# Optimization experiments

Hardware: AMD Instinct MI355X
Metric: run time of the kernel (lower is better)

## Reference

```python
import jax, jax.numpy as jnp
import numpy as np
import math

B, LL, LP = 16, 256, 1024
HID, H = 128, 8
SCALE = math.sqrt(HID)


def setup_inputs() -> dict:
    key = jax.random.key(0)
    ks = jax.random.split(key, 20)
    s = 0.02
    inp = {
        "ligand": jax.random.normal(ks[0], (B, LL, HID), jnp.float32),
        "prot": jax.random.normal(ks[1], (B, LP, HID), jnp.float32),
        "inter": jax.random.uniform(ks[2], (B, 1, LL, LP), jnp.float32),
        # projection weights stored as [in, out] (x @ W + b)
        "Wl1": jax.random.normal(ks[3], (HID, HID * H), jnp.float32) * s,
        "bl1": jnp.zeros((HID * H,), jnp.float32),
        "Wl2": jax.random.normal(ks[4], (HID, HID * H), jnp.float32) * s,
        "bl2": jnp.zeros((HID * H,), jnp.float32),
        "Wp1": jax.random.normal(ks[5], (HID, HID * H), jnp.float32) * s,
        "bp1": jnp.zeros((HID * H,), jnp.float32),
        "Wp2": jax.random.normal(ks[6], (HID, HID * H), jnp.float32) * s,
        "bp2": jnp.zeros((HID * H,), jnp.float32),
        "W11": jax.random.normal(ks[7], (HID * H, HID), jnp.float32) * s,
        "b11": jnp.zeros((HID,), jnp.float32),
        "W12": jax.random.normal(ks[8], (2 * HID, HID), jnp.float32) * s,
        "b12": jnp.zeros((HID,), jnp.float32),
        "W21": jax.random.normal(ks[9], (HID * H, HID), jnp.float32) * s,
        "b21": jnp.zeros((HID,), jnp.float32),
        "W22": jax.random.normal(ks[10], (2 * HID, HID), jnp.float32) * s,
        "b22": jnp.zeros((HID,), jnp.float32),
    }
    return inp


def _heads(x):
    # [B, L, H*D] -> [B, H, L, D]
    b, l, _ = x.shape
    return x.reshape(b, l, H, HID).transpose(0, 2, 1, 3)


def reference(ligand, prot, inter, Wl1, bl1, Wl2, bl2, Wp1, bp1, Wp2, bp2,
              W11, b11, W12, b12, W21, b21, W22, b22):
    relu = jax.nn.relu
    l1 = _heads(relu(ligand @ Wl1 + bl1))   # [B,H,LL,D]
    l2 = _heads(relu(ligand @ Wl2 + bl2))   # [B,H,LL,D]
    p1 = _heads(relu(prot @ Wp1 + bp1))     # [B,H,LP,D]
    p2 = _heads(relu(prot @ Wp2 + bp2))     # [B,H,LP,D]

    energy = jnp.einsum('bhld,bhpd->bhlp', l1, p1) / SCALE
    att = jax.nn.softmax(energy * inter, axis=-1)  # dropout is identity at eval

    # ligand branch: att @ prot2 -> [B,LL,H*D]
    lig3 = jnp.einsum('bhlp,bhpd->blhd', att, p2).reshape(B, LL, H * HID)
    lig3 = jnp.concatenate([lig3 @ W11 + b11, ligand], axis=2)
    lig3 = relu(lig3 @ W12 + b12)

    # protein branch: att^T @ ligand2 -> [B,LP,H*D]
    prot3 = jnp.einsum('bhlp,bhld->bphd', att, l2).reshape(B, LP, H * HID)
    prot3 = jnp.concatenate([prot3 @ W21 + b21, prot], axis=2)
    prot3 = relu(prot3 @ W22 + b22)
    return (lig3, prot3)
```

## Files before the change

### kernel.cpp

```cpp
#include <hip/hip_runtime.h>
#include <hip/hip_bf16.h>

typedef unsigned short u16;
typedef __attribute__((ext_vector_type(4))) float f32x4;
typedef __attribute__((ext_vector_type(4))) unsigned int u32x4;
typedef __attribute__((ext_vector_type(4))) unsigned short u16x4;
typedef __attribute__((ext_vector_type(8))) unsigned short u16x8;
typedef __attribute__((ext_vector_type(8))) __bf16 bf16x8;

__device__ inline float u2f(u16 u) {
    union { unsigned int i; float f; } x; x.i = ((unsigned int)u) << 16; return x.f;
}
__device__ inline u16 f2u(float f) {
    __hip_bfloat16 b = __float2bfloat16(f);
    return *reinterpret_cast<u16*>(&b);
}
__device__ inline f32x4 mfma16(bf16x8 a, bf16x8 b, f32x4 c) {
    return __builtin_amdgcn_mfma_f32_16x16x32_bf16(a, b, c, 0, 0, 0);
}
__device__ inline void gload_lds16(const u16* g, u16* l) {
    __builtin_amdgcn_global_load_lds(
        (const __attribute__((address_space(1))) unsigned int*)g,
        (__attribute__((address_space(3))) unsigned int*)l, 16, 0, 0);
}

__global__ __launch_bounds__(256)
void proj_kernel(const u16* __restrict__ ligb, const u16* __restrict__ protb,
                 const u16* __restrict__ Wl1t, const u16* __restrict__ Wl2t,
                 const u16* __restrict__ Wp1t, const u16* __restrict__ Wp2t,
                 const float* __restrict__ bl1, const float* __restrict__ bl2,
                 const float* __restrict__ bp1, const float* __restrict__ bp2,
                 u16* __restrict__ l1v, u16* __restrict__ l2tv,
                 u16* __restrict__ p1v, u16* __restrict__ p2tv)
{
    __shared__ __align__(16) u16 As[128 * 64];
    __shared__ __align__(16) u16 Bs[128 * 64];
    const int y = blockIdx.y;
    const u16* A; const u16* B; const float* bias; u16* Out;
    int mode, logL, my;
    if (y < 32)       { A = ligb;  B = Wl1t; bias = bl1; Out = l1v;  mode = 1; logL = 8;  my = y; }
    else if (y < 64)  { A = ligb;  B = Wl2t; bias = bl2; Out = l2tv; mode = 3; logL = 8;  my = y - 32; }
    else if (y < 192) { A = protb; B = Wp1t; bias = bp1; Out = p1v;  mode = 1; logL = 10; my = y - 64; }
    else              { A = protb; B = Wp2t; bias = bp2; Out = p2tv; mode = 3; logL = 10; my = y - 192; }
    const int n0 = blockIdx.x * 128, m0 = my * 128;
    const int tid = threadIdx.x;
    const int w = tid >> 6, lane = tid & 63, q = lane >> 4, li = lane & 15;
    const int wr = w >> 1, wc = w & 1;

    const int srow = tid >> 3;
    const int cg = (tid & 7) ^ (srow & 7);
    const int ldsbase = ((tid >> 6) * 8) * 64;

    f32x4 acc[4][4];
    #pragma unroll
    for (int i = 0; i < 4; i++)
        #pragma unroll
        for (int j = 0; j < 4; j++) acc[i][j] = (f32x4){0.f, 0.f, 0.f, 0.f};

    #pragma unroll
    for (int kt = 0; kt < 128; kt += 64) {
        const u16* Ab = A + (long)m0 * 128 + kt + cg * 8;
        const u16* Bb = B + (long)n0 * 128 + kt + cg * 8;
        #pragma unroll
        for (int c = 0; c < 4; c++) {
            gload_lds16(Ab + (long)(c * 32 + srow) * 128, &As[ldsbase + c * 32 * 64]);
            gload_lds16(Bb + (long)(c * 32 + srow) * 128, &Bs[ldsbase + c * 32 * 64]);
        }
        __syncthreads();
        #pragma unroll
        for (int s = 0; s < 2; s++) {
            const int cp = ((s * 4 + q) ^ (li & 7)) * 8;
            bf16x8 av[4], bv[4];
            #pragma unroll
            for (int i = 0; i < 4; i++)
                av[i] = *(bf16x8*)&As[(wr * 64 + i * 16 + li) * 64 + cp];
            #pragma unroll
            for (int j = 0; j < 4; j++)
                bv[j] = *(bf16x8*)&Bs[(wc * 64 + j * 16 + li) * 64 + cp];
            #pragma unroll
            for (int i = 0; i < 4; i++)
                #pragma unroll
                for (int j = 0; j < 4; j++)
                    acc[i][j] = mfma16(av[i], bv[j], acc[i][j]);
        }
        __syncthreads();
    }

    const int Lm = (1 << logL) - 1;
    #pragma unroll
    for (int i = 0; i < 4; i++) {
        #pragma unroll
        for (int j = 0; j < 4; j++) {
            const int col = n0 + wc * 64 + j * 16 + li;
            const float bvs = bias[col];
            if (mode == 3) {
                const int row0 = m0 + wr * 64 + i * 16 + q * 4;
                long base = ((long)(((row0 >> logL) * 8 + (col >> 7)) * 128
                            + (col & 127)) << logL) + (row0 & Lm);
                u16x4 o;
                #pragma unroll
                for (int r = 0; r < 4; r++)
                    o[r] = f2u(fmaxf(acc[i][j][r] + bvs, 0.f));
                *(u16x4*)(Out + base) = o;
            } else {
                #pragma unroll
                for (int r = 0; r < 4; r++) {
                    const int row = m0 + wr * 64 + i * 16 + q * 4 + r;
                    long addr = ((long)((row >> logL) * 8 + (col >> 7)) << (logL + 7))
                              + ((long)(row & Lm) << 7) + (col & 127);
                    Out[addr] = f2u(fmaxf(acc[i][j][r] + bvs, 0.f));
                }
            }
        }
    }
}

__global__ __launch_bounds__(512)
void av_kernel(const u16* __restrict__ att, const u16* __restrict__ p2t,
               const u16* __restrict__ l2t,
               u16* __restrict__ lig3, u16* __restrict__ prot3)
{
    __shared__ __align__(16) u16 As[256 * 64];
    __shared__ __align__(16) u16 Bs[128 * 64];
    __shared__ __align__(16) u16 T[64 * 256];
    const int bid = blockIdx.x;
    const int tid = threadIdx.x;
    const int w = tid >> 6, lane = tid & 63, q = lane >> 4, li = lane & 15;
    const int wr = w >> 1, wc = w & 1;

    f32x4 acc[4][4];
    #pragma unroll
    for (int i = 0; i < 4; i++)
        #pragma unroll
        for (int j = 0; j < 4; j++) acc[i][j] = (f32x4){0.f, 0.f, 0.f, 0.f};

    if (bid < 128) {
        const int bh = bid;
        const u16* A = att + (long)bh * 262144;
        const u16* B = p2t + (long)bh * 131072;
        const int srow = tid >> 3;
        const int cg = (tid & 7) ^ (srow & 7);
        const int ldsbase = ((tid >> 6) * 8) * 64;

        for (int kt = 0; kt < 1024; kt += 64) {
            const u16* Ab = A + kt + cg * 8;
            const u16* Bb = B + kt + cg * 8;
            #pragma unroll
            for (int c = 0; c < 4; c++)
                gload_lds16(Ab + (long)(c * 64 + srow) * 1024,
                            &As[ldsbase + c * 64 * 64]);
            #pragma unroll
            for (int c = 0; c < 2; c++)
                gload_lds16(Bb + (long)(c * 64 + srow) * 1024,
                            &Bs[ldsbase + c * 64 * 64]);
            __syncthreads();
            #pragma unroll
            for (int s = 0; s < 2; s++) {
                const int cp = ((s * 4 + q) ^ (li & 7)) * 8;
                bf16x8 av[4], bv[4];
                #pragma unroll
                for (int i = 0; i < 4; i++)
                    av[i] = *(bf16x8*)&As[(wr * 64 + i * 16 + li) * 64 + cp];
                #pragma unroll
                for (int j = 0; j < 4; j++)
                    bv[j] = *(bf16x8*)&Bs[(wc * 64 + j * 16 + li) * 64 + cp];
                #pragma unroll
                for (int i = 0; i < 4; i++)
                    #pragma unroll
                    for (int j = 0; j < 4; j++)
                        acc[i][j] = mfma16(av[i], bv[j], acc[i][j]);
            }
            __syncthreads();
        }

        const long obase = ((long)(bh >> 3) * 256) * 1024 + (long)(bh & 7) * 128;
        #pragma unroll
        for (int i = 0; i < 4; i++)
            #pragma unroll
            for (int j = 0; j < 4; j++) {
                const int col = wc * 64 + j * 16 + li;
                #pragma unroll
                for (int r = 0; r < 4; r++) {
                    const int row = wr * 64 + i * 16 + q * 4 + r;
                    lig3[obase + (long)row * 1024 + col] = f2u(acc[i][j][r]);
                }
            }
    } else {
        const int pb = bid - 128;
        const int bh = pb >> 2;
        const int m0 = (pb & 3) * 256;
        const u16* A = att + (long)bh * 262144;
        const u16* B = l2t + (long)bh * 32768;
        const int w6 = tid >> 6;
        const int i5 = (tid >> 5) & 1;
        const int srow = tid >> 3;
        const int cg = (tid & 7) ^ (srow & 7);
        const int bldsbase = w6 * 8 * 64;

        for (int kt = 0; kt < 256; kt += 64) {
            #pragma unroll
            for (int c = 0; c < 4; c++) {
                gload_lds16(A + (long)(kt + w6 * 8 + c * 2 + i5) * 1024
                              + m0 + (tid & 31) * 8,
                            &T[w6 * 2048 + c * 512]);
            }
            #pragma unroll
            for (int c = 0; c < 2; c++)
                gload_lds16(B + (long)(c * 64 + srow) * 256 + kt + cg * 8,
                            &Bs[bldsbase + c * 64 * 64]);
            __syncthreads();

            #pragma unroll
            for (int pass = 0; pass < 4; pass++) {
                const int p = pass * 64 + (tid & 63);
                union { u16 e[8]; u32x4 v; } tmp;
                #pragma unroll
                for (int e = 0; e < 8; e++)
                    tmp.e[e] = T[(w6 * 8 + e) * 256 + p];
                *(u32x4*)&As[p * 64 + ((w6 ^ (p & 7)) * 8)] = tmp.v;
            }
            __syncthreads();

            #pragma unroll
            for (int s = 0; s < 2; s++) {
                const int cp = ((s * 4 + q) ^ (li & 7)) * 8;
                bf16x8 av[4], bv[4];
                #pragma unroll
                for (int i = 0; i < 4; i++)
                    av[i] = *(bf16x8*)&As[(wr * 64 + i * 16 + li) * 64 + cp];
                #pragma unroll
                for (int j = 0; j < 4; j++)
                    bv[j] = *(bf16x8*)&Bs[(wc * 64 + j * 16 + li) * 64 + cp];
                #pragma unroll
                for (int i = 0; i < 4; i++)
                    #pragma unroll
                    for (int j = 0; j < 4; j++)
                        acc[i][j] = mfma16(av[i], bv[j], acc[i][j]);
            }
            __syncthreads();
        }

        const long obase = ((long)(bh >> 3) * 1024 + m0) * 1024 + (long)(bh & 7) * 128;
        #pragma unroll
        for (int i = 0; i < 4; i++)
            #pragma unroll
            for (int j = 0; j < 4; j++) {
                const int col = wc * 64 + j * 16 + li;
                #pragma unroll
                for (int r = 0; r < 4; r++) {
                    const int row = wr * 64 + i * 16 + q * 4 + r;
                    prot3[obase + (long)row * 1024 + col] = f2u(acc[i][j][r]);
                }
            }
    }
}

__global__ __launch_bounds__(256)
void finals_kernel(const u16* __restrict__ lig3, const u16* __restrict__ ligb,
                   const u16* __restrict__ WstL, const float* __restrict__ bcL,
                   float* __restrict__ out0,
                   const u16* __restrict__ prot3, const u16* __restrict__ protb,
                   const u16* __restrict__ WstP, const float* __restrict__ bcP,
                   float* __restrict__ out1)
{
    __shared__ __align__(16) u16 As[128 * 64];
    __shared__ __align__(16) u16 Bs[128 * 64];
    const int y = blockIdx.y;
    const u16 *A, *A2, *B; const float* bias; float* Out; int my;
    if (y < 32) { A = lig3;  A2 = ligb;  B = WstL; bias = bcL; Out = out0; my = y; }
    else        { A = prot3; A2 = protb; B = WstP; bias = bcP; Out = out1; my = y - 32; }
    const int m0 = my * 128;
    const int tid = threadIdx.x;
    const int w = tid >> 6, lane = tid & 63, q = lane >> 4, li = lane & 15;
    const int wr = w >> 1, wc = w & 1;

    const int srow = tid >> 3;
    const int cg = (tid & 7) ^ (srow & 7);
    const int ldsbase = ((tid >> 6) * 8) * 64;

    f32x4 acc[4][4];
    #pragma unroll
    for (int i = 0; i < 4; i++)
        #pragma unroll
        for (int j = 0; j < 4; j++) acc[i][j] = (f32x4){0.f, 0.f, 0.f, 0.f};

    for (int kt = 0; kt < 1152; kt += 64) {
        const u16* Abase; long lda; int ktA;
        if (kt >= 1024) { Abase = A2; lda = 128; ktA = kt - 1024; }
        else            { Abase = A;  lda = 1024; ktA = kt; }
        const u16* Ab = Abase + (long)m0 * lda + ktA + cg * 8;
        const u16* Bb = B + kt + cg * 8;
        #pragma unroll
        for (int c = 0; c < 4; c++) {
            gload_lds16(Ab + (long)(c * 32 + srow) * lda,  &As[ldsbase + c * 32 * 64]);
            gload_lds16(Bb + (long)(c * 32 + srow) * 1152, &Bs[ldsbase + c * 32 * 64]);
        }
        __syncthreads();
        #pragma unroll
        for (int s = 0; s < 2; s++) {
            const int cp = ((s * 4 + q) ^ (li & 7)) * 8;
            bf16x8 av[4], bv[4];
            #pragma unroll
            for (int i = 0; i < 4; i++)
                av[i] = *(bf16x8*)&As[(wr * 64 + i * 16 + li) * 64 + cp];
            #pragma unroll
            for (int j = 0; j < 4; j++)
                bv[j] = *(bf16x8*)&Bs[(wc * 64 + j * 16 + li) * 64 + cp];
            #pragma unroll
            for (int i = 0; i < 4; i++)
                #pragma unroll
                for (int j = 0; j < 4; j++)
                    acc[i][j] = mfma16(av[i], bv[j], acc[i][j]);
        }
        __syncthreads();
    }

    #pragma unroll
    for (int i = 0; i < 4; i++)
        #pragma unroll
        for (int j = 0; j < 4; j++) {
            const int col = wc * 64 + j * 16 + li;
            const float bvs = bias[col];
            #pragma unroll
            for (int r = 0; r < 4; r++) {
                const int row = m0 + wr * 64 + i * 16 + q * 4 + r;
                Out[(long)row * 128 + col] = fmaxf(acc[i][j][r] + bvs, 0.f);
            }
        }
}

__global__ __launch_bounds__(512, 4)
void attn_kernel(const u16* __restrict__ l1, const u16* __restrict__ p1,
                 const u16* __restrict__ interb, u16* __restrict__ att)
{
    __shared__ __align__(16) u16 S[32 * 1024];
    __shared__ __align__(16) u16 Bs[2][64 * 64];
    const int id = blockIdx.x;
    const int bh = (id & 7) * 16 + (id >> 6);
    const int mt = (id >> 3) & 7;
    const int b  = bh >> 3;
    const int m0 = mt * 32;
    const int tid = threadIdx.x;
    const float rscale = 0.08838834764831845f;

    {
        const int w = tid >> 6, lane = tid & 63, q = lane >> 4, li = lane & 15;
        const int rgrp = w >> 2, pc = w & 3;
        const int srow = tid >> 3;
        const int cg = (tid & 7) ^ (srow & 7);
        bf16x8 af[4];
        const u16* lp = l1 + ((long)bh * 256 + m0 + rgrp * 16 + li) * 128 + q * 8;
        #pragma unroll
        for (int s = 0; s < 4; s++) af[s] = *(const bf16x8*)(lp + s * 32);
        const int sw = (rgrp * 4 + q) << 4;
        const u16* pbase = p1 + ((long)bh * 1024 + srow) * 128 + cg * 8;
        u16* ldst = &Bs[0][(tid >> 6) * 8 * 64];

        for (int pt = 0; pt < 16; pt++) {
            gload_lds16(pbase + (long)pt * 8192,      ldst);
            gload_lds16(pbase + (long)pt * 8192 + 64, ldst + 64 * 64);
            __syncthreads();
            f32x4 acc = (f32x4){0.f, 0.f, 0.f, 0.f};
            #pragma unroll
            for (int ks = 0; ks < 4; ks++) {
                bf16x8 bv = *(bf16x8*)&Bs[ks >> 1][(pc * 16 + li) * 64
                              + ((((ks & 1) * 4 + q) ^ (li & 7)) * 8)];
                acc = mfma16(af[ks], bv, acc);
            }
            const int col = pt * 64 + pc * 16 + li;
            const int lr0 = rgrp * 16 + q * 4;
            #pragma unroll
            for (int r = 0; r < 4; r++)
                S[((lr0 + r) << 10) + (col ^ sw)] = f2u(acc[r] * rscale);
            __syncthreads();
        }
    }

    const int row = tid >> 4;
    const int lj  = tid & 15;
    const int l   = m0 + row;
    const int sw2 = (row >> 2) << 4;
    const u16* ib = interb + ((long)b * 256 + l) * 1024;

    float mx = -1e30f;
    #pragma unroll
    for (int blk = 0; blk < 8; blk++) {
        const int c = blk * 128 + lj * 8;
        u16* sp = &S[(row << 10) + (c ^ sw2)];
        u16x8 s8 = *(u16x8*)sp;
        u16x8 i8 = *(const u16x8*)(ib + c);
        u16x8 o8;
        #pragma unroll
        for (int e = 0; e < 8; e++) {
            float v = u2f(s8[e]) * u2f(i8[e]);
            mx = fmaxf(mx, v);
            o8[e] = f2u(v);
        }
        *(u16x8*)sp = o8;
    }
    #pragma unroll
    for (int d = 1; d < 16; d <<= 1) mx = fmaxf(mx, __shfl_xor(mx, d, 64));

    float z = 0.f;
    #pragma unroll
    for (int blk = 0; blk < 8; blk++) {
        const int c = blk * 128 + lj * 8;
        u16x8 p8 = *(u16x8*)&S[(row << 10) + (c ^ sw2)];
        #pragma unroll
        for (int e = 0; e < 8; e++) z += __expf(u2f(p8[e]) - mx);
    }
    #pragma unroll
    for (int d = 1; d < 16; d <<= 1) z += __shfl_xor(z, d, 64);
    const float inv = 1.f / z;

    u16* op = att + ((long)bh * 256 + l) * 1024;
    #pragma unroll
    for (int blk = 0; blk < 8; blk++) {
        const int c = blk * 128 + lj * 8;
        u16x8 p8 = *(u16x8*)&S[(row << 10) + (c ^ sw2)];
        u16x8 o8;
        #pragma unroll
        for (int e = 0; e < 8; e++)
            o8[e] = f2u(__expf(u2f(p8[e]) - mx) * inv);
        *(u16x8*)(op + c) = o8;
    }
}

struct TPF { const float* src; u16* dst; int R; int C; };
struct TPF8 { TPF t[8]; };

__global__ __launch_bounds__(256)
void cvtw_kernel(TPF8 args)
{
    TPF tp = args.t[blockIdx.z];
    const int c0 = blockIdx.x * 32, r0 = blockIdx.y * 32;
    if (c0 >= tp.C || r0 >= tp.R) return;
    __shared__ u16 tile[32][33];
    const int tx = threadIdx.x & 31, ty = threadIdx.x >> 5;
    #pragma unroll
    for (int i = 0; i < 4; i++)
        tile[ty + i * 8][tx] = f2u(tp.src[(long)(r0 + ty + i * 8) * tp.C + c0 + tx]);
    __syncthreads();
    #pragma unroll
    for (int i = 0; i < 4; i++)
        tp.dst[(long)(c0 + ty + i * 8) * tp.R + r0 + tx] = tile[tx][ty + i * 8];
}

__global__ __launch_bounds__(256)
void wcomb_kernel(const u16* __restrict__ Wm0, const u16* __restrict__ Wo0,
                  const float* __restrict__ bm0, const float* __restrict__ bo0,
                  u16* __restrict__ Wst0, float* __restrict__ bc0,
                  const u16* __restrict__ Wm1, const u16* __restrict__ Wo1,
                  const float* __restrict__ bm1, const float* __restrict__ bo1,
                  u16* __restrict__ Wst1, float* __restrict__ bc1)
{
    const int zz = blockIdx.y;
    const u16* Wm = zz ? Wm1 : Wm0;
    const u16* Wo = zz ? Wo1 : Wo0;
    const float* bmid = zz ? bm1 : bm0;
    const float* bout = zz ? bo1 : bo0;
    u16* Wst = zz ? Wst1 : Wst0;
    float* bc = zz ? bc1 : bc0;
    const int n = blockIdx.x;
    const int tid = threadIdx.x;
    __shared__ float wrow[128];
    if (tid < 128) wrow[tid] = u2f(Wo[n * 256 + tid]);
    __syncthreads();
    for (int k = tid; k < 1024; k += 256) {
        float acc = 0.f;
        #pragma unroll 4
        for (int j = 0; j < 128; j++) acc += wrow[j] * u2f(Wm[(long)j * 1024 + k]);
        Wst[(long)n * 1152 + k] = f2u(acc);
    }
    if (tid < 128) Wst[(long)n * 1152 + 1024 + tid] = Wo[n * 256 + 128 + tid];
    if (tid == 0) {
        float acc = bout[n];
        for (int j = 0; j < 128; j++) acc += bmid[j] * wrow[j];
        bc[n] = acc;
    }
}

__global__ __launch_bounds__(256)
void cvt3_kernel(const float* __restrict__ a, u16* __restrict__ da, int na,
                 const float* __restrict__ b, u16* __restrict__ db, int nb,
                 const float* __restrict__ c, u16* __restrict__ dc, int nc)
{
    const int zz = blockIdx.y;
    const float* s = zz == 0 ? a : (zz == 1 ? b : c);
    u16* d = zz == 0 ? da : (zz == 1 ? db : dc);
    const int n = zz == 0 ? na : (zz == 1 ? nb : nc);
    const int i = (blockIdx.x * 256 + threadIdx.x) * 4;
    if (i >= n) return;
    const float4 v = *(const float4*)(s + i);
    u16x4 o;
    o.x = f2u(v.x); o.y = f2u(v.y); o.z = f2u(v.z); o.w = f2u(v.w);
    *(u16x4*)(d + i) = o;
}

extern "C" void kernel_launch(void* const* d_in, const int* in_sizes, int n_in,
                              void* d_out, int out_size, void* d_ws, size_t ws_size,
                              hipStream_t stream)
{
    (void)in_sizes; (void)n_in; (void)out_size; (void)ws_size;
    const float* ligand = (const float*)d_in[0];
    const float* prot   = (const float*)d_in[1];
    const float* inter  = (const float*)d_in[2];
    const float* Wl1 = (const float*)d_in[3];  const float* bl1 = (const float*)d_in[4];
    const float* Wl2 = (const float*)d_in[5];  const float* bl2 = (const float*)d_in[6];
    const float* Wp1 = (const float*)d_in[7];  const float* bp1 = (const float*)d_in[8];
    const float* Wp2 = (const float*)d_in[9];  const float* bp2 = (const float*)d_in[10];
    const float* W11 = (const float*)d_in[11]; const float* b11 = (const float*)d_in[12];
    const float* W12 = (const float*)d_in[13]; const float* b12 = (const float*)d_in[14];
    const float* W21 = (const float*)d_in[15]; const float* b21 = (const float*)d_in[16];
    const float* W22 = (const float*)d_in[17]; const float* b22 = (const float*)d_in[18];

    float* out0 = (float*)d_out;
    float* out1 = out0 + (size_t)16 * 256 * 128;

    u16* ws = (u16*)d_ws;
    size_t off = 0;
    auto alloc = [&](size_t n) { u16* p = ws + off; off += n; return p; };
    u16* ligb  = alloc(524288);
    u16* protb = alloc(2097152);
    u16* l1v   = alloc(4194304);
    u16* l2t   = alloc(4194304);
    u16* p1v   = alloc(16777216);
    u16* p2t   = alloc(16777216);
    u16* attv  = alloc(33554432);
    u16* lig3  = alloc(4194304);
    u16* prot3 = alloc(16777216);
    u16* Wl1t  = alloc(131072);
    u16* Wl2t  = alloc(131072);
    u16* Wp1t  = alloc(131072);
    u16* Wp2t  = alloc(131072);
    u16* W11t  = alloc(131072);
    u16* W21t  = alloc(131072);
    u16* W12t  = alloc(32768);
    u16* W22t  = alloc(32768);
    u16* WstL  = alloc(147456);
    u16* WstP  = alloc(147456);
    float* bcL = (float*)alloc(256);
    float* bcP = (float*)alloc(256);

    u16* interb = lig3;

    cvt3_kernel<<<dim3(4096, 3), 256, 0, stream>>>(
        ligand, ligb, 524288, prot, protb, 2097152, inter, interb, 4194304);

    TPF8 tp;
    tp.t[0] = {Wl1, Wl1t, 128, 1024};
    tp.t[1] = {Wl2, Wl2t, 128, 1024};
    tp.t[2] = {Wp1, Wp1t, 128, 1024};
    tp.t[3] = {Wp2, Wp2t, 128, 1024};
    tp.t[4] = {W11, W11t, 1024, 128};
    tp.t[5] = {W21, W21t, 1024, 128};
    tp.t[6] = {W12, W12t, 256, 128};
    tp.t[7] = {W22, W22t, 256, 128};
    cvtw_kernel<<<dim3(32, 32, 8), 256, 0, stream>>>(tp);

    wcomb_kernel<<<dim3(128, 2), 256, 0, stream>>>(
        W11t, W12t, b11, b12, WstL, bcL,
        W21t, W22t, b21, b22, WstP, bcP);

    proj_kernel<<<dim3(8, 320), 256, 0, stream>>>(
        ligb, protb, Wl1t, Wl2t, Wp1t, Wp2t,
        bl1, bl2, bp1, bp2, l1v, l2t, p1v, p2t);

    attn_kernel<<<dim3(1024), 512, 0, stream>>>(l1v, p1v, interb, attv);

    av_kernel<<<dim3(640), 512, 0, stream>>>(attv, p2t, l2t, lig3, prot3);

    finals_kernel<<<dim3(1, 160), 256, 0, stream>>>(
        lig3, ligb, WstL, bcL, out0,
        prot3, protb, WstP, bcP, out1);
}
```

Measured before the change: 282.5 us.

## Load P1 fragments directly to registers in attention score stage, drop LDS staging

```diff
diff --git a/kernel.cpp b/kernel.cpp
--- a/kernel.cpp
+++ b/kernel.cpp
@@ -334,7 +334,6 @@
                  const u16* __restrict__ interb, u16* __restrict__ att)
 {
     __shared__ __align__(16) u16 S[32 * 1024];
-    __shared__ __align__(16) u16 Bs[2][64 * 64];
     const int id = blockIdx.x;
     const int bh = (id & 7) * 16 + (id >> 6);
     const int mt = (id >> 3) & 7;
@@ -345,36 +344,38 @@
 
     {
         const int w = tid >> 6, lane = tid & 63, q = lane >> 4, li = lane & 15;
-        const int rgrp = w >> 2, pc = w & 3;
-        const int srow = tid >> 3;
-        const int cg = (tid & 7) ^ (srow & 7);
-        bf16x8 af[4];
-        const u16* lp = l1 + ((long)bh * 256 + m0 + rgrp * 16 + li) * 128 + q * 8;
-        #pragma unroll
-        for (int s = 0; s < 4; s++) af[s] = *(const bf16x8*)(lp + s * 32);
-        const int sw = (rgrp * 4 + q) << 4;
-        const u16* pbase = p1 + ((long)bh * 1024 + srow) * 128 + cg * 8;
-        u16* ldst = &Bs[0][(tid >> 6) * 8 * 64];
-
-        for (int pt = 0; pt < 16; pt++) {
-            gload_lds16(pbase + (long)pt * 8192,      ldst);
-            gload_lds16(pbase + (long)pt * 8192 + 64, ldst + 64 * 64);
-            __syncthreads();
-            f32x4 acc = (f32x4){0.f, 0.f, 0.f, 0.f};
-            #pragma unroll
-            for (int ks = 0; ks < 4; ks++) {
-                bf16x8 bv = *(bf16x8*)&Bs[ks >> 1][(pc * 16 + li) * 64
-                              + ((((ks & 1) * 4 + q) ^ (li & 7)) * 8)];
-                acc = mfma16(af[ks], bv, acc);
-            }
-            const int col = pt * 64 + pc * 16 + li;
-            const int lr0 = rgrp * 16 + q * 4;
-            #pragma unroll
-            for (int r = 0; r < 4; r++)
-                S[((lr0 + r) << 10) + (col ^ sw)] = f2u(acc[r] * rscale);
-            __syncthreads();
-        }
-    }
+        bf16x8 af[2][4];
+        #pragma unroll
+        for (int g = 0; g < 2; g++) {
+            const u16* lp = l1 + ((long)bh * 256 + m0 + g * 16 + li) * 128 + q * 8;
+            #pragma unroll
+            for (int s = 0; s < 4; s++) af[g][s] = *(const bf16x8*)(lp + s * 32);
+        }
+        const u16* bp0 = p1 + ((long)bh * 1024 + w * 128 + li) * 128 + q * 8;
+        #pragma unroll
+        for (int pf = 0; pf < 8; pf++) {
+            const u16* bp = bp0 + (long)pf * 2048;
+            bf16x8 bv[4];
+            #pragma unroll
+            for (int s = 0; s < 4; s++) bv[s] = *(const bf16x8*)(bp + s * 32);
+            f32x4 acc0 = (f32x4){0.f, 0.f, 0.f, 0.f};
+            f32x4 acc1 = (f32x4){0.f, 0.f, 0.f, 0.f};
+            #pragma unroll
+            for (int s = 0; s < 4; s++) {
+                acc0 = mfma16(af[0][s], bv[s], acc0);
+                acc1 = mfma16(af[1][s], bv[s], acc1);
+            }
+            const int col = w * 128 + pf * 16 + li;
+            #pragma unroll
+            for (int r = 0; r < 4; r++) {
+                const int row0 = q * 4 + r;
+                S[(row0 << 10) + (col ^ ((row0 >> 2) << 4))] = f2u(acc0[r] * rscale);
+                const int row1 = 16 + q * 4 + r;
+                S[(row1 << 10) + (col ^ ((row1 >> 2) << 4))] = f2u(acc1[r] * rscale);
+            }
+        }
+    }
+    __syncthreads();
 
     const int row = tid >> 4;
     const int lj  = tid & 15;
```

Result: slower. 294.1 us (+4.1%).
